# Kernel tuning notes

Hardware: AMD Instinct MI355X
Metric: run time of the kernel (lower is better)

The kernel has to match this reference:

```python
import jax, jax.numpy as jnp
import numpy as np

K, B, N, F, D_CONST = 2, 100000, 1000, 500, 14

def setup_inputs() -> dict:
    key = jax.random.key(0)
    ks = jax.random.split(key, 7)
    height = jax.random.uniform(ks[0], (K, B), dtype=jnp.float32) * 3000.0 + 100.0
    width = jax.random.uniform(ks[1], (K, B), dtype=jnp.float32) * 1.0 + 1.0  # spot width in pixels
    x = jax.random.normal(ks[2], (K, B), dtype=jnp.float32)  # sub-pixel offset from target
    y = jax.random.normal(ks[3], (K, B), dtype=jnp.float32)
    target_locs = jax.random.uniform(ks[4], (N, F, 2), dtype=jnp.float32) * (D_CONST - 1)
    n_idx = jax.random.randint(ks[5], (B,), 0, N)
    f_idx = jax.random.randint(ks[6], (B,), 0, F)
    return {"height": height, "width": width, "x": x, "y": y,
            "target_locs": target_locs, "n_idx": n_idx, "f_idx": f_idx, "D": D_CONST}

def reference(height, width, x, y, target_locs, n_idx, f_idx, D):
    # pixel grid [D, D, 2], 'ij' indexing like torch.meshgrid default
    r = jnp.arange(D, dtype=jnp.float32)
    ii, jj = jnp.meshgrid(r, r, indexing="ij")
    ij_pixel = jnp.stack((ii, jj), axis=-1)  # [D, D, 2]
    # gather target locations and add sub-pixel offsets -> [K, B, 2]
    spot_locs = target_locs[n_idx, f_idx] + jnp.stack((x, y), axis=-1)
    # isotropic 2D Gaussian: MVN with scale_tril = eye(2)*width
    diff = ij_pixel - spot_locs[:, :, None, None, :]  # [K, B, D, D, 2]
    w2 = (width * width)[:, :, None, None]  # [K, B, 1, 1]
    log_prob = -0.5 * jnp.sum(diff * diff, axis=-1) / w2 \
               - jnp.log(2.0 * jnp.pi) - jnp.log(w2)
    gaussian_spot = jnp.exp(log_prob)  # [K, B, D, D]
    return height[:, :, None, None] * gaussian_spot
```

## Files before the change

### kernel.cpp

```cpp
#include <hip/hip_runtime.h>


typedef float f32x4 __attribute__((ext_vector_type(4)));

#define S_SPOTS 25
#define NBLK    (200000 / S_SPOTS)
#define B_NUM   100000u
#define F_NUM   500
#define D_DIM   14u
#define LSTRIDE 16u

__global__ __launch_bounds__(256) void gspot_kernel(
    const float* __restrict__ height,
    const float* __restrict__ width,
    const float* __restrict__ xoff,
    const float* __restrict__ yoff,
    const float* __restrict__ tlocs,
    const int*   __restrict__ n_idx,
    const int*   __restrict__ f_idx,
    f32x4*       __restrict__ out)
{
    __shared__ float sp_sx[S_SPOTS], sp_sy[S_SPOTS], sp_c[S_SPOTS], sp_sc[S_SPOTS];
    __shared__ float ex[S_SPOTS * LSTRIDE];
    __shared__ float ey[S_SPOTS * LSTRIDE];

    const float HALF_LOG2E = 0.7213475204444817f;
    const float INV_2PI    = 0.15915494309189535f;

    const unsigned tid = threadIdx.x;
    const unsigned spot_base = blockIdx.x * S_SPOTS;

    if (tid < S_SPOTS) {
        unsigned spot = spot_base + tid;
        unsigned b    = spot % B_NUM;
        float h  = height[spot];
        float w  = width[spot];
        float sx = xoff[spot];
        float sy = yoff[spot];
        int n = n_idx[b];
        int f = f_idx[b];
        const float* tl = tlocs + ((unsigned)(n * F_NUM + f)) * 2u;
        sx += tl[0];
        sy += tl[1];
        float inv = __builtin_amdgcn_rcpf(w * w);
        sp_sx[tid] = sx;
        sp_sy[tid] = sy;
        sp_c[tid]  = -HALF_LOG2E * inv;
        sp_sc[tid] = h * inv * INV_2PI;
    }
    __syncthreads();

    for (unsigned item = tid; item < S_SPOTS * 2u * D_DIM; item += 256u) {
        unsigned sp = item / (2u * D_DIM);
        unsigned r  = item - sp * (2u * D_DIM);
        float c = sp_c[sp];
        if (r < D_DIM) {
            float d = (float)r - sp_sx[sp];
            ex[sp * LSTRIDE + r] = sp_sc[sp] * __builtin_amdgcn_exp2f(c * d * d);
        } else {
            unsigned j = r - D_DIM;
            float d = (float)j - sp_sy[sp];
            ey[sp * LSTRIDE + j] = __builtin_amdgcn_exp2f(c * d * d);
        }
    }
    __syncthreads();

    f32x4* outb = out + (size_t)spot_base * 49u;
    for (unsigned idx = tid; idx < S_SPOTS * 49u; idx += 256u) {
        unsigned sp = idx / 49u;
        unsigned q  = idx - sp * 49u;
        unsigned p0 = q * 4u;
        const float* exb = ex + sp * LSTRIDE;
        const float* eyb = ey + sp * LSTRIDE;
        f32x4 e;
        #pragma unroll
        for (int m = 0; m < 4; ++m) {
            unsigned p = p0 + (unsigned)m;
            unsigned i = p / D_DIM;
            unsigned j = p - i * D_DIM;
            e[m] = exb[i] * eyb[j];
        }
        outb[idx] = e;
    }
}

extern "C" void kernel_launch(void* const* d_in, const int* in_sizes, int n_in,
                              void* d_out, int out_size, void* d_ws, size_t ws_size,
                              hipStream_t stream) {
    const float* height = (const float*)d_in[0];
    const float* width  = (const float*)d_in[1];
    const float* x      = (const float*)d_in[2];
    const float* y      = (const float*)d_in[3];
    const float* tlocs  = (const float*)d_in[4];
    const int*   n_idx  = (const int*)d_in[5];
    const int*   f_idx  = (const int*)d_in[6];
    f32x4* out = (f32x4*)d_out;

    hipLaunchKernelGGL(gspot_kernel, dim3(NBLK), dim3(256), 0, stream,
                       height, width, x, y, tlocs, n_idx, f_idx, out);
}
```

Measured before the change: 34.54 us.

## Give each wave its own spots and replace block barriers with wave-local waits

Restructures the kernel so each 64-lane wave independently handles 16 spots in a private LDS region. The two __syncthreads barriers become s_waitcnt lgkmcnt plus scheduling barriers, and the loops are fully unrolled with fixed trip counts. Block size in spots goes from 25 to 64, which reduces the grid size. This removes cross-wave barrier stalls and leftover-iteration imbalance, but it relies on wave-synchronous LDS visibility, which is not guaranteed by the HIP programming model.

```diff
diff --git a/kernel.cpp b/kernel.cpp
--- a/kernel.cpp
+++ b/kernel.cpp
@@ -3,12 +3,14 @@
 
 typedef float f32x4 __attribute__((ext_vector_type(4)));
 
-#define S_SPOTS 25
-#define NBLK    (200000 / S_SPOTS)
 #define B_NUM   100000u
 #define F_NUM   500
 #define D_DIM   14u
-#define LSTRIDE 16u
+#define SPW     16u
+#define WPB     4u
+#define SPB     (SPW * WPB)
+#define NBLK    (200000 / SPB)
+#define WREG    576u
 
 __global__ __launch_bounds__(256) void gspot_kernel(
     const float* __restrict__ height,
@@ -20,19 +22,20 @@
     const int*   __restrict__ f_idx,
     f32x4*       __restrict__ out)
 {
-    __shared__ float sp_sx[S_SPOTS], sp_sy[S_SPOTS], sp_c[S_SPOTS], sp_sc[S_SPOTS];
-    __shared__ float ex[S_SPOTS * LSTRIDE];
-    __shared__ float ey[S_SPOTS * LSTRIDE];
+    __shared__ float lds[WPB * WREG];
 
     const float HALF_LOG2E = 0.7213475204444817f;
     const float INV_2PI    = 0.15915494309189535f;
 
-    const unsigned tid = threadIdx.x;
-    const unsigned spot_base = blockIdx.x * S_SPOTS;
+    const unsigned tid  = threadIdx.x;
+    const unsigned wave = tid >> 6;
+    const unsigned lane = tid & 63u;
+    float* wl = &lds[wave * WREG];
+    const unsigned wave_spot0 = blockIdx.x * SPB + wave * SPW;
 
-    if (tid < S_SPOTS) {
-        unsigned spot = spot_base + tid;
-        unsigned b    = spot % B_NUM;
+    if (lane < SPW) {
+        unsigned spot = wave_spot0 + lane;
+        unsigned b    = spot >= B_NUM ? spot - B_NUM : spot;
         float h  = height[spot];
         float w  = width[spot];
         float sx = xoff[spot];
@@ -43,44 +46,52 @@
         sx += tl[0];
         sy += tl[1];
         float inv = __builtin_amdgcn_rcpf(w * w);
-        sp_sx[tid] = sx;
-        sp_sy[tid] = sy;
-        sp_c[tid]  = -HALF_LOG2E * inv;
-        sp_sc[tid] = h * inv * INV_2PI;
+        wl[lane]        = sx;
+        wl[16u + lane]  = sy;
+        wl[32u + lane]  = -HALF_LOG2E * inv;
+        wl[48u + lane]  = h * inv * INV_2PI;
     }
-    __syncthreads();
+    asm volatile("s_waitcnt lgkmcnt(0)" ::: "memory");
+    __builtin_amdgcn_sched_barrier(0);
 
-    for (unsigned item = tid; item < S_SPOTS * 2u * D_DIM; item += 256u) {
-        unsigned sp = item / (2u * D_DIM);
-        unsigned r  = item - sp * (2u * D_DIM);
-        float c = sp_c[sp];
+    #pragma unroll
+    for (unsigned k = 0; k < 7u; ++k) {
+        unsigned item = lane + 64u * k;
+        unsigned sp   = item / 28u;
+        unsigned r    = item - sp * 28u;
+        float c = wl[32u + sp];
         if (r < D_DIM) {
-            float d = (float)r - sp_sx[sp];
-            ex[sp * LSTRIDE + r] = sp_sc[sp] * __builtin_amdgcn_exp2f(c * d * d);
+            float d = (float)r - wl[sp];
+            wl[64u + sp * 16u + r] = wl[48u + sp] * __builtin_amdgcn_exp2f(c * d * d);
         } else {
             unsigned j = r - D_DIM;
-            float d = (float)j - sp_sy[sp];
-            ey[sp * LSTRIDE + j] = __builtin_amdgcn_exp2f(c * d * d);
+            float d = (float)j - wl[16u + sp];
+            wl[320u + sp * 16u + j] = __builtin_amdgcn_exp2f(c * d * d);
         }
     }
-    __syncthreads();
+    asm volatile("s_waitcnt lgkmcnt(0)" ::: "memory");
+    __builtin_amdgcn_sched_barrier(0);
 
-    f32x4* outb = out + (size_t)spot_base * 49u;
-    for (unsigned idx = tid; idx < S_SPOTS * 49u; idx += 256u) {
-        unsigned sp = idx / 49u;
-        unsigned q  = idx - sp * 49u;
-        unsigned p0 = q * 4u;
-        const float* exb = ex + sp * LSTRIDE;
-        const float* eyb = ey + sp * LSTRIDE;
-        f32x4 e;
-        #pragma unroll
-        for (int m = 0; m < 4; ++m) {
-            unsigned p = p0 + (unsigned)m;
-            unsigned i = p / D_DIM;
-            unsigned j = p - i * D_DIM;
-            e[m] = exb[i] * eyb[j];
+    f32x4* op = out + (size_t)wave_spot0 * 49u;
+    #pragma unroll
+    for (unsigned k = 0; k < 13u; ++k) {
+        unsigned idx = lane + 64u * k;
+        if (k < 12u || lane < 16u) {
+            unsigned sp = idx / 49u;
+            unsigned q  = idx - sp * 49u;
+            unsigned p0 = q * 4u;
+            const float* exb = &wl[64u  + sp * 16u];
+            const float* eyb = &wl[320u + sp * 16u];
+            f32x4 e;
+            #pragma unroll
+            for (int m = 0; m < 4; ++m) {
+                unsigned p = p0 + (unsigned)m;
+                unsigned i = p / D_DIM;
+                unsigned j = p - i * D_DIM;
+                e[m] = exb[i] * eyb[j];
+            }
+            op[idx] = e;
         }
-        outb[idx] = e;
     }
 }
 
```

Result: faster. 32.37 us (-6.3%).
